# Optimization experiments

Measured on AMD Instinct MI355X. Metric: run time of the kernel, lower is better.

## Reference

```python
import jax, jax.numpy as jnp
import numpy as np

D_MODEL = 1024
N_HEADS = 8
EDGE_HID = 512
N_EDGE_CLS = 18
N_NODE_CLS = 18
MAX_NODES = 15


def setup_inputs() -> dict:
    key = jax.random.key(0)
    ks = jax.random.split(key, 24)
    B, T, L, D = 32, 4, 1024, D_MODEL
    N = MAX_NODES
    s = 0.02
    visual_feats = jax.random.normal(ks[0], (B, T, L, D), jnp.float32)
    nodes = jax.random.randint(ks[1], (B, N), 0, N_NODE_CLS, dtype=jnp.int32)
    bboxes = jax.random.uniform(ks[2], (B, N, 4), jnp.float32)
    # embedding table; padding_idx=-1 -> last row zeroed (unused due to clamp)
    emb = (jax.random.normal(ks[3], (N_NODE_CLS + 1, D)) * s).at[-1].set(0.0)
    Wb = jax.random.normal(ks[4], (D, 4)) * s
    bb = jnp.zeros((D,), jnp.float32)
    Wq = jax.random.normal(ks[5], (D, D)) * s
    bq = jnp.zeros((D,), jnp.float32)
    Wk = jax.random.normal(ks[6], (D, D)) * s
    bk = jnp.zeros((D,), jnp.float32)
    Wv = jax.random.normal(ks[7], (D, D)) * s
    bv = jnp.zeros((D,), jnp.float32)
    Wo = jax.random.normal(ks[8], (D, D)) * s
    bo = jnp.zeros((D,), jnp.float32)
    W1 = jax.random.normal(ks[9], (EDGE_HID, 2 * D)) * s
    b1 = jnp.zeros((EDGE_HID,), jnp.float32)
    W2 = jax.random.normal(ks[10], (N_EDGE_CLS, EDGE_HID)) * s
    b2 = jnp.zeros((N_EDGE_CLS,), jnp.float32)
    Wh1 = jax.random.normal(ks[11], (256, D)) * s
    bh1 = jnp.zeros((256,), jnp.float32)
    Wh2 = jax.random.normal(ks[12], (1, 256)) * s
    bh2 = jnp.zeros((1,), jnp.float32)
    return dict(visual_feats=visual_feats, nodes=nodes, bboxes=bboxes, emb=emb,
                Wb=Wb, bb=bb, Wq=Wq, bq=bq, Wk=Wk, bk=bk, Wv=Wv, bv=bv,
                Wo=Wo, bo=bo, W1=W1, b1=b1, W2=W2, b2=b2,
                Wh1=Wh1, bh1=bh1, Wh2=Wh2, bh2=bh2)


def reference(visual_feats, nodes, bboxes, emb, Wb, bb, Wq, bq, Wk, bk, Wv, bv,
              Wo, bo, W1, b1, W2, b2, Wh1, bh1, Wh2, bh2):
    B, T, L, D = visual_feats.shape
    H = N_HEADS
    Hd = D // H
    v_f = visual_feats[:, -1]  # (B, L, D)
    n_emb = emb[jnp.maximum(nodes, 0)]            # (B, N, D)
    query = n_emb + bboxes @ Wb.T + bb            # (B, N, D)
    N = query.shape[1]
    # multi-head cross-attention (query=nodes, key/value=visual tokens)
    q = (query @ Wq.T + bq).reshape(B, N, H, Hd)
    k = (v_f @ Wk.T + bk).reshape(B, L, H, Hd)
    v = (v_f @ Wv.T + bv).reshape(B, L, H, Hd)
    scores = jnp.einsum('bnhd,blhd->bhnl', q, k) / jnp.sqrt(jnp.float32(Hd))
    attn = jax.nn.softmax(scores, axis=-1)
    ctx = jnp.einsum('bhnl,blhd->bnhd', attn, v).reshape(B, N, D)
    enriched = ctx @ Wo.T + bo                    # (B, N, D)
    pad = nodes == -1                             # all False here
    clean = jnp.where(pad[..., None], 0.0, enriched)
    # edge MLP: decompose first Linear over the concat into two half matmuls
    h_i = enriched @ W1[:, :D].T                  # (B, N, E)
    h_j = enriched @ W1[:, D:].T                  # (B, N, E)
    pair = jax.nn.relu(h_i[:, :, None, :] + h_j[:, None, :, :] + b1)  # (B,N,N,E)
    edge_logits = pair @ W2.T + b2                # (B, N, N, 18)
    valid = jnp.maximum(jnp.sum(~pad, axis=1, keepdims=True), 1).astype(enriched.dtype)
    gfeat = jnp.sum(clean, axis=1) / valid        # (B, D)
    energy = (jax.nn.relu(gfeat @ Wh1.T + bh1) @ Wh2.T + bh2).squeeze(-1)  # (B,)
    return edge_logits, energy
```

## Files before the change

### kernel.cpp

```cpp
#include <hip/hip_runtime.h>


typedef __attribute__((ext_vector_type(8))) short bf16x8;
typedef __attribute__((ext_vector_type(4))) float f32x4;

__device__ __forceinline__ unsigned short f2bf(float f) {
    unsigned int u = __float_as_uint(f);
    u = u + 0x7FFFu + ((u >> 16) & 1u);
    return (unsigned short)(u >> 16);
}

__device__ __forceinline__ void gload_lds16(const void* g, void* l) {
    __builtin_amdgcn_global_load_lds(
        (const __attribute__((address_space(1))) void*)g,
        (__attribute__((address_space(3))) void*)l,
        16, 0, 0);
}

template <bool OUTBF>
__global__ __launch_bounds__(256) void bfgemm_k(
    const unsigned short* __restrict__ A, const unsigned short* __restrict__ B,
    void* __restrict__ Cv, int M, long sA, long sB, long sC)
{
    const int b  = blockIdx.z;
    const int m0 = blockIdx.y * 64;
    const int n0 = blockIdx.x * 128;
    const unsigned short* Ab = A + b * sA;
    const unsigned short* Bb = B + b * sB;

    __shared__ __align__(16) unsigned short As[64 * 32];
    __shared__ __align__(16) unsigned short Bs[128 * 32];

    const int t    = threadIdx.x;
    const int lane = t & 63;
    const int w    = t >> 6;
    const int wm   = w >> 1, wn = w & 1;

    f32x4 acc[2][4] = {};

    const int ar = t >> 2;
    const int ac = (t & 3) * 8;

    unsigned short* AsW  = As + w * 512;
    unsigned short* BsW0 = Bs + w * 512;
    unsigned short* BsW1 = Bs + 2048 + w * 512;
    const unsigned short* ga  = Ab + (long)(m0 + ar) * 1024 + ac;
    const unsigned short* gb0 = Bb + (long)(n0 + ar) * 1024 + ac;
    const unsigned short* gb1 = Bb + (long)(n0 + 64 + ar) * 1024 + ac;

    for (int k0 = 0; k0 < 1024; k0 += 32) {
        __syncthreads();
        gload_lds16(ga  + k0, AsW);
        gload_lds16(gb0 + k0, BsW0);
        gload_lds16(gb1 + k0, BsW1);
        __syncthreads();

        const int krow = (lane >> 4) * 8;
        bf16x8 af[2], bf[4];
#pragma unroll
        for (int fi = 0; fi < 2; ++fi)
            af[fi] = *(const bf16x8*)&As[(wm * 32 + fi * 16 + (lane & 15)) * 32 + krow];
#pragma unroll
        for (int fj = 0; fj < 4; ++fj)
            bf[fj] = *(const bf16x8*)&Bs[(wn * 64 + fj * 16 + (lane & 15)) * 32 + krow];
#pragma unroll
        for (int fi = 0; fi < 2; ++fi)
#pragma unroll
            for (int fj = 0; fj < 4; ++fj)
                acc[fi][fj] = __builtin_amdgcn_mfma_f32_16x16x32_bf16(
                    af[fi], bf[fj], acc[fi][fj], 0, 0, 0);
    }

    const int rbase = (lane >> 4) * 4;
    const int cn    = n0 + wn * 64 + (lane & 15);
#pragma unroll
    for (int fi = 0; fi < 2; ++fi) {
        const int mb = m0 + wm * 32 + fi * 16 + rbase;
#pragma unroll
        for (int r = 0; r < 4; ++r) {
            const int m = mb + r;
            if (m < M) {
#pragma unroll
                for (int fj = 0; fj < 4; ++fj) {
                    if constexpr (OUTBF)
                        ((unsigned short*)Cv)[b * sC + (long)m * 1024 + cn + fj * 16]
                            = f2bf(acc[fi][fj][r]);
                    else
                        ((float*)Cv)[b * sC + (long)m * 1024 + cn + fj * 16]
                            = acc[fi][fj][r];
                }
            }
        }
    }
}

template <int OM>
__global__ __launch_bounds__(256) void pgemm_k(
    const unsigned short* __restrict__ A, const unsigned short* __restrict__ B,
    const float* __restrict__ bias, float* __restrict__ C,
    unsigned short* __restrict__ Cbf,
    int M, int K, int lda, int ldb, int ldc)
{
    const int m0 = blockIdx.y * 64;
    const int n0 = blockIdx.x * 64;

    __shared__ __align__(16) unsigned short As[64 * 32];
    __shared__ __align__(16) unsigned short Bs[64 * 32];

    const int t    = threadIdx.x;
    const int lane = t & 63;
    const int w    = t >> 6;
    const int wm   = w >> 1, wn = w & 1;
    const int lm   = lane & 15, lg = lane >> 4;

    const int ar = t >> 2;
    const int ac = (t & 3) * 8;

    f32x4 acc[2][2] = {};

    unsigned short* AsW = As + w * 512;
    unsigned short* BsW = Bs + w * 512;
    const unsigned short* ga = A + (long)(m0 + ar) * lda + ac;
    const unsigned short* gb = B + (long)(n0 + ar) * ldb + ac;

    for (int k0 = 0; k0 < K; k0 += 32) {
        __syncthreads();
        gload_lds16(ga + k0, AsW);
        gload_lds16(gb + k0, BsW);
        __syncthreads();

        const int krow = lg * 8 & 24;
        bf16x8 af[2], bf[2];
#pragma unroll
        for (int fi = 0; fi < 2; ++fi)
            af[fi] = *(const bf16x8*)&As[(wm * 32 + fi * 16 + lm) * 32 + krow];
#pragma unroll
        for (int fj = 0; fj < 2; ++fj)
            bf[fj] = *(const bf16x8*)&Bs[(wn * 32 + fj * 16 + lm) * 32 + krow];
#pragma unroll
        for (int fi = 0; fi < 2; ++fi)
#pragma unroll
            for (int fj = 0; fj < 2; ++fj)
                acc[fi][fj] = __builtin_amdgcn_mfma_f32_16x16x32_bf16(
                    af[fi], bf[fj], acc[fi][fj], 0, 0, 0);
    }

    const int rbase = lg * 4;
#pragma unroll
    for (int fi = 0; fi < 2; ++fi) {
        const int mb = m0 + wm * 32 + fi * 16 + rbase;
#pragma unroll
        for (int r = 0; r < 4; ++r) {
            const int m = mb + r;
            if (m < M) {
#pragma unroll
                for (int fj = 0; fj < 2; ++fj) {
                    const int n = n0 + wn * 32 + fj * 16 + lm;
                    float v = acc[fi][fj][r];
                    if (bias) v += bias[n];
                    if constexpr (OM != 2) C[(long)m * ldc + n] = v;
                    if constexpr (OM >= 1) Cbf[(long)m * ldc + n] = f2bf(v);
                }
            }
        }
    }
}

__global__ __launch_bounds__(256) void qw_k(
    const unsigned short* __restrict__ qbf, const unsigned short* __restrict__ WkT,
    unsigned short* __restrict__ qW, float scale)
{
    const int z = blockIdx.y;
    const int b = z >> 3, h = z & 7;
    const int w = threadIdx.x >> 6, lane = threadIdx.x & 63;
    const int lm = lane & 15, lg = lane >> 4;
    const int n0w = blockIdx.x * 256 + w * 64;

    const unsigned short* Ar = qbf + (long)(b * 15 + lm) * 1024 + h * 128 + lg * 8;
    const unsigned short* Br = WkT + (long)(n0w + lm) * 1024 + h * 128 + lg * 8;

    bf16x8 af[4];
#pragma unroll
    for (int ks = 0; ks < 4; ++ks) af[ks] = *(const bf16x8*)(Ar + ks * 32);

    f32x4 acc[4] = {};
#pragma unroll
    for (int fj = 0; fj < 4; ++fj) {
#pragma unroll
        for (int ks = 0; ks < 4; ++ks) {
            bf16x8 bf = *(const bf16x8*)(Br + (long)fj * 16 * 1024 + ks * 32);
            acc[fj] = __builtin_amdgcn_mfma_f32_16x16x32_bf16(af[ks], bf, acc[fj], 0, 0, 0);
        }
    }

#pragma unroll
    for (int r = 0; r < 4; ++r) {
        const int m = lg * 4 + r;
        if (m < 15) {
#pragma unroll
            for (int fj = 0; fj < 4; ++fj)
                qW[(long)b * 131072 + (long)(m * 8 + h) * 1024 + n0w + fj * 16 + lm]
                    = f2bf(acc[fj][r] * scale);
        }
    }
}

__global__ __launch_bounds__(256) void ctx_k(
    const unsigned short* __restrict__ cf, const unsigned short* __restrict__ Wvb,
    const float* __restrict__ bv, unsigned short* __restrict__ ctx)
{
    const int z = blockIdx.x;
    const int b = z >> 3, h = z & 7;
    const int w = threadIdx.x >> 6, lane = threadIdx.x & 63;
    const int lm = lane & 15, lg = lane >> 4;

    const unsigned short* Ar = cf + (long)b * 122880 + (long)(lm * 8 + h) * 1024 + lg * 8;
    const unsigned short* Br = Wvb + (long)(h * 128 + w * 32 + lm) * 1024 + lg * 8;

    f32x4 acc[2] = {};
    for (int k0 = 0; k0 < 1024; k0 += 32) {
        bf16x8 af = *(const bf16x8*)(Ar + k0);
        bf16x8 b0 = *(const bf16x8*)(Br + k0);
        bf16x8 b1 = *(const bf16x8*)(Br + 16 * 1024 + k0);
        acc[0] = __builtin_amdgcn_mfma_f32_16x16x32_bf16(af, b0, acc[0], 0, 0, 0);
        acc[1] = __builtin_amdgcn_mfma_f32_16x16x32_bf16(af, b1, acc[1], 0, 0, 0);
    }

#pragma unroll
    for (int r = 0; r < 4; ++r) {
        const int m = lg * 4 + r;
        if (m < 15) {
#pragma unroll
            for (int fj = 0; fj < 2; ++fj) {
                const int gcol = h * 128 + w * 32 + fj * 16 + lm;
                ctx[(long)(b * 15 + m) * 1024 + gcol] = f2bf(acc[fj][r] + bv[gcol]);
            }
        }
    }
}

__global__ __launch_bounds__(256) void uber_cvt_k(
    const int* __restrict__ nodes, const float* __restrict__ bboxes,
    const float* __restrict__ emb, const float* __restrict__ Wb,
    const float* __restrict__ bb, unsigned short* __restrict__ qbf,
    const float* __restrict__ Wq, const float* __restrict__ Wo,
    const float* __restrict__ Wv, const float* __restrict__ W1,
    const float* __restrict__ Wk,
    unsigned short* __restrict__ dWq, unsigned short* __restrict__ dWo,
    unsigned short* __restrict__ dWv, unsigned short* __restrict__ dW1r,
    unsigned short* __restrict__ dWkT)
{
    __shared__ unsigned short tile[64][72];
    const int bid = blockIdx.x;
    const int t = threadIdx.x;

    if (bid < 4096) {
        const int which = bid >> 10;
        const int i = (bid & 1023) * 256 + t;
        const float* s;
        unsigned short* d;
        if (which == 3) {
            const int flat = i * 4, n = flat >> 10, k = flat & 1023;
            s = (n < 512) ? W1 + (long)n * 2048 + k
                          : W1 + (long)(n - 512) * 2048 + 1024 + k;
            d = dW1r + flat;
        } else {
            s = (which == 0 ? Wq : which == 1 ? Wo : Wv) + (long)i * 4;
            d = (which == 0 ? dWq : which == 1 ? dWo : dWv) + (long)i * 4;
        }
        float4 v = *(const float4*)s;
        ushort4 o;
        o.x = f2bf(v.x); o.y = f2bf(v.y); o.z = f2bf(v.z); o.w = f2bf(v.w);
        *(ushort4*)d = o;
    } else if (bid < 4352) {
        const int tl = bid - 4096;
        const int d0 = (tl >> 4) * 64, e0 = (tl & 15) * 64;
        const int r0 = t >> 4, c0 = (t & 15) * 4;
#pragma unroll
        for (int rr = 0; rr < 4; ++rr) {
            const int r = r0 + rr * 16;
            float4 v = *(const float4*)&Wk[(long)(d0 + r) * 1024 + e0 + c0];
            tile[r][c0 + 0] = f2bf(v.x); tile[r][c0 + 1] = f2bf(v.y);
            tile[r][c0 + 2] = f2bf(v.z); tile[r][c0 + 3] = f2bf(v.w);
        }
        __syncthreads();
#pragma unroll
        for (int rr = 0; rr < 4; ++rr) {
            const int idx = rr * 256 + t;
            const int e = idx >> 4, c4 = (idx & 15) * 4;
            ushort4 o;
            o.x = tile[c4 + 0][e]; o.y = tile[c4 + 1][e];
            o.z = tile[c4 + 2][e]; o.w = tile[c4 + 3][e];
            *(ushort4*)&dWkT[(long)(e0 + e) * 1024 + d0 + c4] = o;
        }
    } else {
        const int blk = bid - 4352;
        const int node = nodes[blk];
        const int idx = node < 0 ? 0 : node;
        const float4 bx = *(const float4*)&bboxes[blk * 4];
        const float* er = emb + (long)idx * 1024;
        for (int d = t; d < 1024; d += 256) {
            const float4 w = *(const float4*)&Wb[d * 4];
            qbf[(long)blk * 1024 + d] = f2bf(
                er[d] + bb[d] + bx.x * w.x + bx.y * w.y + bx.z * w.z + bx.w * w.w);
        }
    }
}

__global__ __launch_bounds__(256) void cvt_k(
    const float* __restrict__ vf, unsigned short* __restrict__ vbf,
    unsigned short* __restrict__ vbfT)
{
    const int b  = blockIdx.z;
    const int e0 = blockIdx.x * 64;
    const int l0 = blockIdx.y * 64;
    const float* src = vf + (long)b * 4194304;
    __shared__ unsigned short tile[64][72];
    const int t = threadIdx.x;
    const int r0 = t >> 4, c0 = (t & 15) * 4;
#pragma unroll
    for (int rr = 0; rr < 4; ++rr) {
        const int r = r0 + rr * 16;
        float4 v = *(const float4*)&src[(long)(l0 + r) * 1024 + e0 + c0];
        ushort4 o;
        o.x = f2bf(v.x); o.y = f2bf(v.y); o.z = f2bf(v.z); o.w = f2bf(v.w);
        tile[r][c0 + 0] = o.x; tile[r][c0 + 1] = o.y;
        tile[r][c0 + 2] = o.z; tile[r][c0 + 3] = o.w;
        *(ushort4*)&vbf[(long)b * 1048576 + (long)(l0 + r) * 1024 + e0 + c0] = o;
    }
    __syncthreads();
#pragma unroll
    for (int rr = 0; rr < 4; ++rr) {
        const int idx = rr * 256 + t;
        const int e   = idx >> 4;
        const int c4  = (idx & 15) * 4;
        ushort4 o;
        o.x = tile[c4 + 0][e]; o.y = tile[c4 + 1][e];
        o.z = tile[c4 + 2][e]; o.w = tile[c4 + 3][e];
        *(ushort4*)&vbfT[(long)b * 1048576 + (long)(e0 + e) * 1024 + l0 + c4] = o;
    }
}

__global__ __launch_bounds__(256) void softmax_k(
    const float* __restrict__ sc, unsigned short* __restrict__ attn)
{
    __shared__ float red[4];
    const int blk = blockIdx.x;
    const int b = blk / 120, r = blk % 120;
    const float* p = sc + (long)blk * 1024;
    const int t = threadIdx.x;
    float4 v = *(const float4*)&p[t * 4];

    float m = fmaxf(fmaxf(v.x, v.y), fmaxf(v.z, v.w));
#pragma unroll
    for (int o = 32; o; o >>= 1) m = fmaxf(m, __shfl_xor(m, o));
    if ((t & 63) == 0) red[t >> 6] = m;
    __syncthreads();
    m = fmaxf(fmaxf(red[0], red[1]), fmaxf(red[2], red[3]));
    __syncthreads();

    v.x = __expf(v.x - m); v.y = __expf(v.y - m);
    v.z = __expf(v.z - m); v.w = __expf(v.w - m);
    float s = v.x + v.y + v.z + v.w;
#pragma unroll
    for (int o = 32; o; o >>= 1) s += __shfl_xor(s, o);
    if ((t & 63) == 0) red[t >> 6] = s;
    __syncthreads();
    s = red[0] + red[1] + red[2] + red[3];
    const float inv = 1.0f / s;
    ushort4 o;
    o.x = f2bf(v.x * inv); o.y = f2bf(v.y * inv);
    o.z = f2bf(v.z * inv); o.w = f2bf(v.w * inv);
    *(ushort4*)&attn[(long)(b * 128 + r) * 1024 + t * 4] = o;
}

__global__ __launch_bounds__(320) void edge_k(
    const float* __restrict__ hh, const float* __restrict__ b1,
    const float* __restrict__ W2, const float* __restrict__ b2,
    float* __restrict__ out)
{
    const int b = blockIdx.x, i = blockIdx.y;
    const int t = threadIdx.x;
    __shared__ float hiS[256];
    __shared__ float b1S[256];
    __shared__ float hjS[15][257];
    __shared__ float w2S[18][257];
    const int j = t / 18, c = t % 18;
    float acc = 0.0f;

    for (int u0 = 0; u0 < 512; u0 += 256) {
        __syncthreads();
        if (t < 64) {
            float4 v = *(const float4*)&hh[(long)(b * 15 + i) * 1024 + u0 + t * 4];
            hiS[t * 4 + 0] = v.x; hiS[t * 4 + 1] = v.y;
            hiS[t * 4 + 2] = v.z; hiS[t * 4 + 3] = v.w;
        } else if (t < 128) {
            const int tt = t - 64;
            float4 v = *(const float4*)&b1[u0 + tt * 4];
            b1S[tt * 4 + 0] = v.x; b1S[tt * 4 + 1] = v.y;
            b1S[tt * 4 + 2] = v.z; b1S[tt * 4 + 3] = v.w;
        }
        for (int x = t; x < 960; x += 320) {
            const int r = x >> 6, cc = (x & 63) * 4;
            float4 v = *(const float4*)&hh[(long)(b * 15 + r) * 1024 + 512 + u0 + cc];
            hjS[r][cc + 0] = v.x; hjS[r][cc + 1] = v.y;
            hjS[r][cc + 2] = v.z; hjS[r][cc + 3] = v.w;
        }
        for (int x = t; x < 1152; x += 320) {
            const int r = x >> 6, cc = (x & 63) * 4;
            float4 v = *(const float4*)&W2[(long)r * 512 + u0 + cc];
            w2S[r][cc + 0] = v.x; w2S[r][cc + 1] = v.y;
            w2S[r][cc + 2] = v.z; w2S[r][cc + 3] = v.w;
        }
        __syncthreads();
        if (t < 270) {
            for (int u = 0; u < 256; ++u) {
                float p = hiS[u] + hjS[j][u] + b1S[u];
                p = p > 0.0f ? p : 0.0f;
                acc += p * w2S[c][u];
            }
        }
    }
    if (t < 270)
        out[((long)(b * 15 + i) * 15 + j) * 18 + c] = acc + b2[c];
}

__global__ __launch_bounds__(256) void energy12_k(
    const float* __restrict__ enr, const int* __restrict__ nodes,
    const float* __restrict__ Wh1, const float* __restrict__ bh1,
    const float* __restrict__ Wh2, float* __restrict__ hidr)
{
    const int b  = blockIdx.y;
    const int u0 = blockIdx.x * 16;
    const int t = threadIdx.x;
    __shared__ float gf[1024];

    int cnt = 0;
#pragma unroll
    for (int n = 0; n < 15; ++n) cnt += (nodes[b * 15 + n] != -1) ? 1 : 0;
    const float inv_valid = 1.0f / fmaxf((float)cnt, 1.0f);
    for (int e = t; e < 1024; e += 256) {
        float s = 0.0f;
#pragma unroll
        for (int n = 0; n < 15; ++n) {
            const bool ok = nodes[b * 15 + n] != -1;
            s += ok ? enr[(long)(b * 15 + n) * 1024 + e] : 0.0f;
        }
        gf[e] = s * inv_valid;
    }
    __syncthreads();

    const int wave = t >> 6, lane = t & 63;
#pragma unroll
    for (int r = 0; r < 4; ++r) {
        const int u = u0 + wave * 4 + r;
        float s = 0.0f;
#pragma unroll
        for (int e0 = 0; e0 < 1024; e0 += 64)
            s += gf[e0 + lane] * Wh1[(long)u * 1024 + e0 + lane];
#pragma unroll
        for (int o = 32; o; o >>= 1) s += __shfl_xor(s, o);
        if (lane == 0)
            hidr[b * 256 + u] = fmaxf(s + bh1[u], 0.0f) * Wh2[u];
    }
}

__global__ __launch_bounds__(256) void energy3_k(
    const float* __restrict__ hidr, const float* __restrict__ bh2,
    float* __restrict__ out)
{
    const int b = blockIdx.x;
    const int t = threadIdx.x;
    __shared__ float red[4];
    float v = hidr[b * 256 + t];
#pragma unroll
    for (int o = 32; o; o >>= 1) v += __shfl_xor(v, o);
    if ((t & 63) == 0) red[t >> 6] = v;
    __syncthreads();
    if (t == 0) out[129600 + b] = red[0] + red[1] + red[2] + red[3] + bh2[0];
}

extern "C" void kernel_launch(void* const* d_in, const int* in_sizes, int n_in,
                              void* d_out, int out_size, void* d_ws, size_t ws_size,
                              hipStream_t stream)
{
    const float* visual = (const float*)d_in[0];
    const int*   nodes  = (const int*)  d_in[1];
    const float* bboxes = (const float*)d_in[2];
    const float* emb    = (const float*)d_in[3];
    const float* Wb     = (const float*)d_in[4];
    const float* bb     = (const float*)d_in[5];
    const float* Wq     = (const float*)d_in[6];
    const float* bq     = (const float*)d_in[7];
    const float* Wk     = (const float*)d_in[8];
    const float* Wv     = (const float*)d_in[10];
    const float* bv     = (const float*)d_in[11];
    const float* Wo     = (const float*)d_in[12];
    const float* bo     = (const float*)d_in[13];
    const float* W1     = (const float*)d_in[14];
    const float* b1     = (const float*)d_in[15];
    const float* W2     = (const float*)d_in[16];
    const float* b2     = (const float*)d_in[17];
    const float* Wh1    = (const float*)d_in[18];
    const float* bh1    = (const float*)d_in[19];
    const float* Wh2    = (const float*)d_in[20];
    const float* bh2    = (const float*)d_in[21];

    float* out = (float*)d_out;
    float* ws  = (float*)d_ws;

    unsigned short* query_bf = (unsigned short*)(ws);
    unsigned short* q_bf     = (unsigned short*)(ws + 131072);
    float* scores = ws + 262144;
    unsigned short* ctxf_bf  = (unsigned short*)(ws + 4194304);
    unsigned short* ctx_bf   = (unsigned short*)(ws + 6160384);
    float* enr    = ws + 6422528;
    unsigned short* enr_bf   = (unsigned short*)(ws + 6914048);
    float* hh     = ws + 7176192;
    unsigned short* Wq_bf  = (unsigned short*)(ws + 7667712);
    unsigned short* Wo_bf  = (unsigned short*)(ws + 8192000);
    unsigned short* Wv_bf  = (unsigned short*)(ws + 8716288);
    unsigned short* W1r_bf = (unsigned short*)(ws + 9240576);
    unsigned short* WkT_bf = (unsigned short*)(ws + 9764864);
    unsigned short* qW_bf   = (unsigned short*)(ws + 10289152);
    unsigned short* attn_bf = (unsigned short*)(ws + 12386304);
    unsigned short* v_bf    = (unsigned short*)(ws + 14483456);
    unsigned short* v_bfT   = (unsigned short*)(ws + 31260672);
    float* hidr   = ws + 48070656;

    const float inv_sqrt_hd = 0.08838834764831845f;
    const float* v_f = visual + 3 * 1048576;

    uber_cvt_k<<<4832, 256, 0, stream>>>(
        nodes, bboxes, emb, Wb, bb, query_bf,
        Wq, Wo, Wv, W1, Wk, Wq_bf, Wo_bf, Wv_bf, W1r_bf, WkT_bf);
    cvt_k<<<dim3(16, 16, 32), 256, 0, stream>>>(v_f, v_bf, v_bfT);

    pgemm_k<2><<<dim3(16, 8), 256, 0, stream>>>(
        query_bf, Wq_bf, bq, nullptr, q_bf, 480, 1024, 1024, 1024, 1024);

    qw_k<<<dim3(4, 256), 256, 0, stream>>>(q_bf, WkT_bf, qW_bf, inv_sqrt_hd);

    bfgemm_k<false><<<dim3(8, 2, 32), 256, 0, stream>>>(
        qW_bf, v_bf, scores, 120, 131072, 1048576, 122880);

    softmax_k<<<3840, 256, 0, stream>>>(scores, attn_bf);

    bfgemm_k<true><<<dim3(8, 2, 32), 256, 0, stream>>>(
        attn_bf, v_bfT, ctxf_bf, 120, 131072, 1048576, 122880);

    ctx_k<<<256, 256, 0, stream>>>(ctxf_bf, Wv_bf, bv, ctx_bf);

    pgemm_k<1><<<dim3(16, 8), 256, 0, stream>>>(
        ctx_bf, Wo_bf, bo, enr, enr_bf, 480, 1024, 1024, 1024, 1024);

    pgemm_k<0><<<dim3(16, 8), 256, 0, stream>>>(
        enr_bf, W1r_bf, nullptr, hh, nullptr, 480, 1024, 1024, 1024, 1024);

    edge_k<<<dim3(32, 15), 320, 0, stream>>>(hh, b1, W2, b2, out);

    energy12_k<<<dim3(16, 32), 256, 0, stream>>>(enr, nodes, Wh1, bh1, Wh2, hidr);
    energy3_k<<<32, 256, 0, stream>>>(hidr, bh2, out);
}
```

Baseline: 238.4 us.

## Fuse fp32-to-bf16 conversion of visual feats into the scores GEMM; merge tail kernels

The scores GEMM now reads the fp32 visual features directly and converts them to bf16 while staging into LDS. This removes the separate row-major bf16 copy of V, which cut about 64MB of writes and 64MB of later reads. The transpose conversion kernel still runs, but it now writes only the transposed copy. The edge MLP and energy hidden-layer kernels are merged into one launch to save a kernel launch. In exchange, the scores GEMM loads fp32 data through registers instead of direct-to-LDS loads, which may expose more load latency.

```diff
diff --git a/kernel.cpp b/kernel.cpp
--- a/kernel.cpp
+++ b/kernel.cpp
@@ -17,10 +17,9 @@
         16, 0, 0);
 }
 
-template <bool OUTBF>
 __global__ __launch_bounds__(256) void bfgemm_k(
     const unsigned short* __restrict__ A, const unsigned short* __restrict__ B,
-    void* __restrict__ Cv, int M, long sA, long sB, long sC)
+    unsigned short* __restrict__ C, int M, long sA, long sB, long sC)
 {
     const int b  = blockIdx.z;
     const int m0 = blockIdx.y * 64;
@@ -81,14 +80,88 @@
             const int m = mb + r;
             if (m < M) {
 #pragma unroll
-                for (int fj = 0; fj < 4; ++fj) {
-                    if constexpr (OUTBF)
-                        ((unsigned short*)Cv)[b * sC + (long)m * 1024 + cn + fj * 16]
-                            = f2bf(acc[fi][fj][r]);
-                    else
-                        ((float*)Cv)[b * sC + (long)m * 1024 + cn + fj * 16]
-                            = acc[fi][fj][r];
-                }
+                for (int fj = 0; fj < 4; ++fj)
+                    C[b * sC + (long)m * 1024 + cn + fj * 16] = f2bf(acc[fi][fj][r]);
+            }
+        }
+    }
+}
+
+__global__ __launch_bounds__(256) void sgemm_k(
+    const unsigned short* __restrict__ A, const float* __restrict__ Bf,
+    float* __restrict__ C, int M, long sA, long sB, long sC)
+{
+    const int b  = blockIdx.z;
+    const int m0 = blockIdx.y * 64;
+    const int n0 = blockIdx.x * 128;
+    const unsigned short* Ab = A + b * sA;
+    const float* Bb = Bf + b * sB;
+    float* Cb = C + b * sC;
+
+    __shared__ __align__(16) unsigned short As[64 * 32];
+    __shared__ __align__(16) unsigned short Bs[128 * 32];
+
+    const int t    = threadIdx.x;
+    const int lane = t & 63;
+    const int w    = t >> 6;
+    const int wm   = w >> 1, wn = w & 1;
+
+    f32x4 acc[2][4] = {};
+
+    const int ar = t >> 2;
+    const int ac = (t & 3) * 8;
+
+    unsigned short* AsW = As + w * 512;
+    const unsigned short* ga = Ab + (long)(m0 + ar) * 1024 + ac;
+    const float* gb0 = Bb + (long)(n0 + ar) * 1024 + ac;
+    const float* gb1 = Bb + (long)(n0 + 64 + ar) * 1024 + ac;
+
+    for (int k0 = 0; k0 < 1024; k0 += 32) {
+        float4 v0a = *(const float4*)(gb0 + k0);
+        float4 v0b = *(const float4*)(gb0 + k0 + 4);
+        float4 v1a = *(const float4*)(gb1 + k0);
+        float4 v1b = *(const float4*)(gb1 + k0 + 4);
+        __syncthreads();
+        gload_lds16(ga + k0, AsW);
+        ushort4 o;
+        o.x = f2bf(v0a.x); o.y = f2bf(v0a.y); o.z = f2bf(v0a.z); o.w = f2bf(v0a.w);
+        *(ushort4*)&Bs[t * 8] = o;
+        o.x = f2bf(v0b.x); o.y = f2bf(v0b.y); o.z = f2bf(v0b.z); o.w = f2bf(v0b.w);
+        *(ushort4*)&Bs[t * 8 + 4] = o;
+        o.x = f2bf(v1a.x); o.y = f2bf(v1a.y); o.z = f2bf(v1a.z); o.w = f2bf(v1a.w);
+        *(ushort4*)&Bs[2048 + t * 8] = o;
+        o.x = f2bf(v1b.x); o.y = f2bf(v1b.y); o.z = f2bf(v1b.z); o.w = f2bf(v1b.w);
+        *(ushort4*)&Bs[2048 + t * 8 + 4] = o;
+        __syncthreads();
+
+        const int krow = (lane >> 4) * 8;
+        bf16x8 af[2], bf[4];
+#pragma unroll
+        for (int fi = 0; fi < 2; ++fi)
+            af[fi] = *(const bf16x8*)&As[(wm * 32 + fi * 16 + (lane & 15)) * 32 + krow];
+#pragma unroll
+        for (int fj = 0; fj < 4; ++fj)
+            bf[fj] = *(const bf16x8*)&Bs[(wn * 64 + fj * 16 + (lane & 15)) * 32 + krow];
+#pragma unroll
+        for (int fi = 0; fi < 2; ++fi)
+#pragma unroll
+            for (int fj = 0; fj < 4; ++fj)
+                acc[fi][fj] = __builtin_amdgcn_mfma_f32_16x16x32_bf16(
+                    af[fi], bf[fj], acc[fi][fj], 0, 0, 0);
+    }
+
+    const int rbase = (lane >> 4) * 4;
+    const int cn    = n0 + wn * 64 + (lane & 15);
+#pragma unroll
+    for (int fi = 0; fi < 2; ++fi) {
+        const int mb = m0 + wm * 32 + fi * 16 + rbase;
+#pragma unroll
+        for (int r = 0; r < 4; ++r) {
+            const int m = mb + r;
+            if (m < M) {
+#pragma unroll
+                for (int fj = 0; fj < 4; ++fj)
+                    Cb[(long)m * 1024 + cn + fj * 16] = acc[fi][fj][r];
             }
         }
     }
@@ -307,9 +380,8 @@
     }
 }
 
-__global__ __launch_bounds__(256) void cvt_k(
-    const float* __restrict__ vf, unsigned short* __restrict__ vbf,
-    unsigned short* __restrict__ vbfT)
+__global__ __launch_bounds__(256) void cvtT_k(
+    const float* __restrict__ vf, unsigned short* __restrict__ vbfT)
 {
     const int b  = blockIdx.z;
     const int e0 = blockIdx.x * 64;
@@ -322,11 +394,8 @@
     for (int rr = 0; rr < 4; ++rr) {
         const int r = r0 + rr * 16;
         float4 v = *(const float4*)&src[(long)(l0 + r) * 1024 + e0 + c0];
-        ushort4 o;
-        o.x = f2bf(v.x); o.y = f2bf(v.y); o.z = f2bf(v.z); o.w = f2bf(v.w);
-        tile[r][c0 + 0] = o.x; tile[r][c0 + 1] = o.y;
-        tile[r][c0 + 2] = o.z; tile[r][c0 + 3] = o.w;
-        *(ushort4*)&vbf[(long)b * 1048576 + (long)(l0 + r) * 1024 + e0 + c0] = o;
+        tile[r][c0 + 0] = f2bf(v.x); tile[r][c0 + 1] = f2bf(v.y);
+        tile[r][c0 + 2] = f2bf(v.z); tile[r][c0 + 3] = f2bf(v.w);
     }
     __syncthreads();
 #pragma unroll
@@ -374,94 +443,99 @@
     *(ushort4*)&attn[(long)(b * 128 + r) * 1024 + t * 4] = o;
 }
 
-__global__ __launch_bounds__(320) void edge_k(
+__global__ __launch_bounds__(320) void tail_k(
     const float* __restrict__ hh, const float* __restrict__ b1,
     const float* __restrict__ W2, const float* __restrict__ b2,
-    float* __restrict__ out)
-{
-    const int b = blockIdx.x, i = blockIdx.y;
-    const int t = threadIdx.x;
-    __shared__ float hiS[256];
-    __shared__ float b1S[256];
-    __shared__ float hjS[15][257];
-    __shared__ float w2S[18][257];
-    const int j = t / 18, c = t % 18;
-    float acc = 0.0f;
-
-    for (int u0 = 0; u0 < 512; u0 += 256) {
-        __syncthreads();
-        if (t < 64) {
-            float4 v = *(const float4*)&hh[(long)(b * 15 + i) * 1024 + u0 + t * 4];
-            hiS[t * 4 + 0] = v.x; hiS[t * 4 + 1] = v.y;
-            hiS[t * 4 + 2] = v.z; hiS[t * 4 + 3] = v.w;
-        } else if (t < 128) {
-            const int tt = t - 64;
-            float4 v = *(const float4*)&b1[u0 + tt * 4];
-            b1S[tt * 4 + 0] = v.x; b1S[tt * 4 + 1] = v.y;
-            b1S[tt * 4 + 2] = v.z; b1S[tt * 4 + 3] = v.w;
-        }
-        for (int x = t; x < 960; x += 320) {
-            const int r = x >> 6, cc = (x & 63) * 4;
-            float4 v = *(const float4*)&hh[(long)(b * 15 + r) * 1024 + 512 + u0 + cc];
-            hjS[r][cc + 0] = v.x; hjS[r][cc + 1] = v.y;
-            hjS[r][cc + 2] = v.z; hjS[r][cc + 3] = v.w;
-        }
-        for (int x = t; x < 1152; x += 320) {
-            const int r = x >> 6, cc = (x & 63) * 4;
-            float4 v = *(const float4*)&W2[(long)r * 512 + u0 + cc];
-            w2S[r][cc + 0] = v.x; w2S[r][cc + 1] = v.y;
-            w2S[r][cc + 2] = v.z; w2S[r][cc + 3] = v.w;
-        }
-        __syncthreads();
-        if (t < 270) {
-            for (int u = 0; u < 256; ++u) {
-                float p = hiS[u] + hjS[j][u] + b1S[u];
-                p = p > 0.0f ? p : 0.0f;
-                acc += p * w2S[c][u];
-            }
-        }
-    }
-    if (t < 270)
-        out[((long)(b * 15 + i) * 15 + j) * 18 + c] = acc + b2[c];
-}
-
-__global__ __launch_bounds__(256) void energy12_k(
     const float* __restrict__ enr, const int* __restrict__ nodes,
     const float* __restrict__ Wh1, const float* __restrict__ bh1,
-    const float* __restrict__ Wh2, float* __restrict__ hidr)
-{
-    const int b  = blockIdx.y;
-    const int u0 = blockIdx.x * 16;
+    const float* __restrict__ Wh2, float* __restrict__ hidr,
+    float* __restrict__ out)
+{
+    __shared__ float sm[8993];
+    const int bid = blockIdx.x;
     const int t = threadIdx.x;
-    __shared__ float gf[1024];
-
-    int cnt = 0;
-#pragma unroll
-    for (int n = 0; n < 15; ++n) cnt += (nodes[b * 15 + n] != -1) ? 1 : 0;
-    const float inv_valid = 1.0f / fmaxf((float)cnt, 1.0f);
-    for (int e = t; e < 1024; e += 256) {
-        float s = 0.0f;
-#pragma unroll
-        for (int n = 0; n < 15; ++n) {
-            const bool ok = nodes[b * 15 + n] != -1;
-            s += ok ? enr[(long)(b * 15 + n) * 1024 + e] : 0.0f;
-        }
-        gf[e] = s * inv_valid;
-    }
-    __syncthreads();
-
-    const int wave = t >> 6, lane = t & 63;
-#pragma unroll
-    for (int r = 0; r < 4; ++r) {
-        const int u = u0 + wave * 4 + r;
-        float s = 0.0f;
-#pragma unroll
-        for (int e0 = 0; e0 < 1024; e0 += 64)
-            s += gf[e0 + lane] * Wh1[(long)u * 1024 + e0 + lane];
-#pragma unroll
-        for (int o = 32; o; o >>= 1) s += __shfl_xor(s, o);
-        if (lane == 0)
-            hidr[b * 256 + u] = fmaxf(s + bh1[u], 0.0f) * Wh2[u];
+
+    if (bid < 480) {
+        const int b = bid / 15, i = bid % 15;
+        float* hiS = sm;
+        float* b1S = sm + 256;
+        float* hjS = sm + 512;
+        float* w2S = sm + 512 + 3855;
+        const int j = t / 18, c = t % 18;
+        float acc = 0.0f;
+
+        for (int u0 = 0; u0 < 512; u0 += 256) {
+            __syncthreads();
+            if (t < 64) {
+                float4 v = *(const float4*)&hh[(long)(b * 15 + i) * 1024 + u0 + t * 4];
+                hiS[t * 4 + 0] = v.x; hiS[t * 4 + 1] = v.y;
+                hiS[t * 4 + 2] = v.z; hiS[t * 4 + 3] = v.w;
+            } else if (t < 128) {
+                const int tt = t - 64;
+                float4 v = *(const float4*)&b1[u0 + tt * 4];
+                b1S[tt * 4 + 0] = v.x; b1S[tt * 4 + 1] = v.y;
+                b1S[tt * 4 + 2] = v.z; b1S[tt * 4 + 3] = v.w;
+            }
+            for (int x = t; x < 960; x += 320) {
+                const int r = x >> 6, cc = (x & 63) * 4;
+                float4 v = *(const float4*)&hh[(long)(b * 15 + r) * 1024 + 512 + u0 + cc];
+                hjS[r * 257 + cc + 0] = v.x; hjS[r * 257 + cc + 1] = v.y;
+                hjS[r * 257 + cc + 2] = v.z; hjS[r * 257 + cc + 3] = v.w;
+            }
+            for (int x = t; x < 1152; x += 320) {
+                const int r = x >> 6, cc = (x & 63) * 4;
+                float4 v = *(const float4*)&W2[(long)r * 512 + u0 + cc];
+                w2S[r * 257 + cc + 0] = v.x; w2S[r * 257 + cc + 1] = v.y;
+                w2S[r * 257 + cc + 2] = v.z; w2S[r * 257 + cc + 3] = v.w;
+            }
+            __syncthreads();
+            if (t < 270) {
+                for (int u = 0; u < 256; ++u) {
+                    float p = hiS[u] + hjS[j * 257 + u] + b1S[u];
+                    p = p > 0.0f ? p : 0.0f;
+                    acc += p * w2S[c * 257 + u];
+                }
+            }
+        }
+        if (t < 270)
+            out[((long)(bid) * 15 + j) * 18 + c] = acc + b2[c];
+    } else {
+        const int z = bid - 480;
+        const int u0 = (z & 15) * 16;
+        const int b  = z >> 4;
+        float* gf = sm;
+
+        int cnt = 0;
+#pragma unroll
+        for (int n = 0; n < 15; ++n) cnt += (nodes[b * 15 + n] != -1) ? 1 : 0;
+        const float inv_valid = 1.0f / fmaxf((float)cnt, 1.0f);
+        if (t < 256) {
+            for (int e = t; e < 1024; e += 256) {
+                float s = 0.0f;
+#pragma unroll
+                for (int n = 0; n < 15; ++n) {
+                    const bool ok = nodes[b * 15 + n] != -1;
+                    s += ok ? enr[(long)(b * 15 + n) * 1024 + e] : 0.0f;
+                }
+                gf[e] = s * inv_valid;
+            }
+        }
+        __syncthreads();
+        if (t < 256) {
+            const int wave = t >> 6, lane = t & 63;
+#pragma unroll
+            for (int r = 0; r < 4; ++r) {
+                const int u = u0 + wave * 4 + r;
+                float s = 0.0f;
+#pragma unroll
+                for (int e0 = 0; e0 < 1024; e0 += 64)
+                    s += gf[e0 + lane] * Wh1[(long)u * 1024 + e0 + lane];
+#pragma unroll
+                for (int o = 32; o; o >>= 1) s += __shfl_xor(s, o);
+                if (lane == 0)
+                    hidr[b * 256 + u] = fmaxf(s + bh1[u], 0.0f) * Wh2[u];
+            }
+        }
     }
 }
 
@@ -524,7 +598,6 @@
     unsigned short* WkT_bf = (unsigned short*)(ws + 9764864);
     unsigned short* qW_bf   = (unsigned short*)(ws + 10289152);
     unsigned short* attn_bf = (unsigned short*)(ws + 12386304);
-    unsigned short* v_bf    = (unsigned short*)(ws + 14483456);
     unsigned short* v_bfT   = (unsigned short*)(ws + 31260672);
     float* hidr   = ws + 48070656;
 
@@ -534,19 +607,20 @@
     uber_cvt_k<<<4832, 256, 0, stream>>>(
         nodes, bboxes, emb, Wb, bb, query_bf,
         Wq, Wo, Wv, W1, Wk, Wq_bf, Wo_bf, Wv_bf, W1r_bf, WkT_bf);
-    cvt_k<<<dim3(16, 16, 32), 256, 0, stream>>>(v_f, v_bf, v_bfT);
 
     pgemm_k<2><<<dim3(16, 8), 256, 0, stream>>>(
         query_bf, Wq_bf, bq, nullptr, q_bf, 480, 1024, 1024, 1024, 1024);
 
     qw_k<<<dim3(4, 256), 256, 0, stream>>>(q_bf, WkT_bf, qW_bf, inv_sqrt_hd);
 
-    bfgemm_k<false><<<dim3(8, 2, 32), 256, 0, stream>>>(
-        qW_bf, v_bf, scores, 120, 131072, 1048576, 122880);
+    sgemm_k<<<dim3(8, 2, 32), 256, 0, stream>>>(
+        qW_bf, v_f, scores, 120, 131072, 4194304, 122880);
+
+    cvtT_k<<<dim3(16, 16, 32), 256, 0, stream>>>(v_f, v_bfT);
 
     softmax_k<<<3840, 256, 0, stream>>>(scores, attn_bf);
 
-    bfgemm_k<true><<<dim3(8, 2, 32), 256, 0, stream>>>(
+    bfgemm_k<<<dim3(8, 2, 32), 256, 0, stream>>>(
         attn_bf, v_bfT, ctxf_bf, 120, 131072, 1048576, 122880);
 
     ctx_k<<<256, 256, 0, stream>>>(ctxf_bf, Wv_bf, bv, ctx_bf);
@@ -557,8 +631,8 @@
     pgemm_k<0><<<dim3(16, 8), 256, 0, stream>>>(
         enr_bf, W1r_bf, nullptr, hh, nullptr, 480, 1024, 1024, 1024, 1024);
 
-    edge_k<<<dim3(32, 15), 320, 0, stream>>>(hh, b1, W2, b2, out);
-
-    energy12_k<<<dim3(16, 32), 256, 0, stream>>>(enr, nodes, Wh1, bh1, Wh2, hidr);
+    tail_k<<<992, 320, 0, stream>>>(
+        hh, b1, W2, b2, enr, nodes, Wh1, bh1, Wh2, hidr, out);
+
     energy3_k<<<32, 256, 0, stream>>>(hidr, bh2, out);
 }
```

Result: faster. 215.9 us, median of 2 (-9.5%).
